# Kernel tuning notes

Measured on AMD Instinct MI355X. Metric: run time of the kernel, lower is better.

## Reference

```python
import jax, jax.numpy as jnp
import numpy as np

H = 28; W = 28; N = H * W
P = N              # padded max persistence pairs per homology dimension
T = 32             # landscape resolution
K1, K2 = 2, 3      # K_max for the two topo layers
M0_1, M0_2 = 0.05, 0.2
LIMS = ((1.0, 28.0), (1.0, 28.0))


def _make_nbrs(h, w, conn8):
    idx = np.arange(h * w).reshape(h, w)
    offs = [(-1, 0), (1, 0), (0, -1), (0, 1)]
    if conn8:
        offs += [(-1, -1), (-1, 1), (1, -1), (1, 1)]
    nbrs = []
    for i in range(h):
        for j in range(w):
            cur = [idx[i + a, j + b] for a, b in offs if 0 <= i + a < h and 0 <= j + b < w]
            nbrs.append(np.asarray(cur, np.int64))
    return nbrs

_NBR4 = _make_nbrs(H, W, False)
_NBR8 = _make_nbrs(H, W, True)


def _h0_pairs(vals, nbrs):
    # 0-dim persistence pairs of a vertex-valued sublevel filtration (union-find, elder rule)
    order = np.argsort(vals, kind="stable")
    pos = np.empty(N, np.int64); pos[order] = np.arange(N)
    parent = np.arange(N); birth = np.arange(N)
    added = np.zeros(N, bool)
    bi = np.zeros(P, np.int32); di = np.zeros(P, np.int32)
    k = 0
    def find(x):
        r = x
        while parent[r] != r: r = parent[r]
        while parent[x] != r: parent[x], x = r, parent[x]
        return r
    for v in order:
        added[v] = True
        for u in nbrs[v]:
            if not added[u]: continue
            ru, rv = find(u), find(v)
            if ru == rv: continue
            if pos[birth[ru]] <= pos[birth[rv]]:
                lb = birth[rv]; parent[rv] = ru
            else:
                lb = birth[ru]; parent[ru] = rv
            if k < P:
                bi[k] = lb; di[k] = v; k += 1
    return bi, di


def _pers_pairs_np(x):
    # x: [M, N] -> (birth_idx, death_idx) each [M, 2, P]; padded pairs point at idx 0 (zero persistence)
    x = np.asarray(x, np.float64)
    M = x.shape[0]
    bi = np.zeros((M, 2, P), np.int32); di = np.zeros((M, 2, P), np.int32)
    for m in range(M):
        b0, d0 = _h0_pairs(x[m], _NBR4)      # H0: sublevel, 4-connectivity
        b1, d1 = _h0_pairs(-x[m], _NBR8)     # H1 by Alexander duality: H0 of superlevel, 8-connectivity
        bi[m, 0], di[m, 0] = b0, d0
        bi[m, 1], di[m, 1] = d1, b1          # H1 birth = vals[d1], death = vals[b1]
    return bi, di


def _grid_d2():
    xs = np.linspace(LIMS[0][0], LIMS[0][1], H)
    ys = np.linspace(LIMS[1][0], LIMS[1][1], W)
    gx, gy = np.meshgrid(xs, ys, indexing="ij")
    pts = np.stack([gx.ravel(), gy.ravel()], 1)              # [N, 2] grid coordinates
    d2 = ((pts[:, None, :] - pts[None, :, :]) ** 2).sum(-1)  # [N, N] squared distances
    si = np.argsort(d2, axis=1, kind="stable")
    return jnp.asarray(si), jnp.asarray(np.take_along_axis(d2, si, 1), jnp.float32)

_SORT_IDX, _D2S = _grid_d2()


def dtm(x_flat, m0):
    # weighted distance-to-measure on the pixel grid, r=2; x_flat: [M, N] positive weights
    bound = m0 * jnp.sum(x_flat, -1, keepdims=True)                        # [M, 1]
    ws = x_flat[:, _SORT_IDX]                                              # [M, N, N] weights in distance order
    cum = jnp.cumsum(ws, -1)
    eff = jnp.minimum(jnp.maximum(bound[..., None] - (cum - ws), 0.0), ws) # effective mass per neighbor
    return jnp.sqrt(jnp.sum(eff * _D2S, -1) / bound)                       # [M, N]


def _landscape(vals, bi, di, start, end, K):
    # persistence landscape lambda_k sampled on T points from (birth, death) critical-vertex indices
    M = vals.shape[0]
    mi = jnp.arange(M)[:, None, None]
    b = vals[mi, bi]; d = vals[mi, di]                                     # [M, 2, P]
    t = jnp.linspace(start, end, T, dtype=vals.dtype)                      # [T]
    tent = jnp.maximum(jnp.minimum(t - b[..., None], d[..., None] - t), 0.0)  # [M, 2, P, T]
    lam, _ = jax.lax.top_k(jnp.swapaxes(tent, -1, -2), K)                  # [M, 2, T, K]
    return jnp.swapaxes(lam, -1, -2).reshape(M, 2 * K * T)                 # [M, dims*K*T]


def pl_features(vals, start, end, K):
    M = vals.shape[0]
    bi, di = jax.pure_callback(
        _pers_pairs_np,
        (jax.ShapeDtypeStruct((M, 2, P), np.int32),
         jax.ShapeDtypeStruct((M, 2, P), np.int32)),
        jax.lax.stop_gradient(vals))
    return _landscape(vals, bi, di, start, end, K)


def setup_inputs():
    key = jax.random.key(0)
    ks = jax.random.split(key, 7)
    B = 64
    return {
        "input": jax.random.uniform(ks[0], (B, 1, H, W), jnp.float32, 1e-3, 1.0),
        "w_g1": 0.1 * jax.random.normal(ks[1], (32, 2 * K1 * T), jnp.float32),
        "b_g1": 0.1 * jax.random.normal(ks[2], (32,), jnp.float32),
        "w_g2": 0.1 * jax.random.normal(ks[3], (32, 2 * K2 * T), jnp.float32),
        "b_g2": 0.1 * jax.random.normal(ks[4], (32,), jnp.float32),
        "w_fc": 0.1 * jax.random.normal(ks[5], (10, 64), jnp.float32),
        "b_fc": 0.1 * jax.random.normal(ks[6], (10,), jnp.float32),
    }


def reference(input, w_g1, b_g1, w_g2, b_g2, w_fc, b_fc):
    x_flat = input.reshape(-1, N)                                        # num_channels = 1
    f1 = dtm(x_flat, M0_1)
    f2 = dtm(x_flat, M0_2)
    x1 = jax.nn.relu(pl_features(f1, 0.0, 7.0, K1) @ w_g1.T + b_g1)      # topo layer 1 (start=0, end=7, K=2)
    x2 = jax.nn.relu(pl_features(f2, 1.0, 8.0, K2) @ w_g2.T + b_g2)      # topo layer 2 (start=1, end=8, K=3)
    return jnp.concatenate([x1, x2], -1) @ w_fc.T + b_fc                 # [B, num_classes]
```

## Files before the change

### kernel.cpp

```cpp
#include <hip/hip_runtime.h>

#define HW 28
#define NPIX 784
#define NIMG 64
#define MAXD2 1459
#define MAXREC 5504

#define DXPK 41048u
#define DYPK 34949u

__global__ void xt_sums_kernel(const float* __restrict__ x,
                               float* __restrict__ sums,
                               float* __restrict__ xT) {
    int tid = threadIdx.x;
    int m = blockIdx.x;
    const float* xr = x + m * NPIX;
    float acc = 0.f;
    for (int j = tid; j < NPIX; j += 256) {
        float v = xr[j];
        xT[j * NIMG + m] = v;
        acc += v;
    }
    for (int off = 32; off > 0; off >>= 1) acc += __shfl_down(acc, off, 64);
    __shared__ float red[4];
    int lane = tid & 63, w = tid >> 6;
    if (lane == 0) red[w] = acc;
    __syncthreads();
    if (tid == 0) sums[m] = red[0] + red[1] + red[2] + red[3];
}

__global__ void sortdtm_kernel(const float* __restrict__ x,
                               const float* __restrict__ xT,
                               const float* __restrict__ sums,
                               float* __restrict__ F) {
    __shared__ int cnt[MAXD2];
    __shared__ int d2v[NPIX];
    __shared__ unsigned int tpl[NPIX];
    __shared__ int wtot[4];
    int tid = threadIdx.x;
    int i = blockIdx.x;

    for (int b = tid; b < MAXD2; b += 256) cnt[b] = 0;
    __syncthreads();
    int ii = i / HW, ij = i % HW;
    for (int j = tid; j < NPIX; j += 256) {
        int di = ii - j / HW, dj = ij - j % HW;
        int d = di * di + dj * dj;
        d2v[j] = d;
        atomicAdd(&cnt[d], 1);
    }
    __syncthreads();
    int b0 = tid * 6;
    int lc[6];
    int s0 = 0;
    #pragma unroll
    for (int t = 0; t < 6; ++t) {
        int b = b0 + t;
        lc[t] = (b < MAXD2) ? cnt[b] : 0;
        s0 += lc[t];
    }
    int lane = tid & 63, wv = tid >> 6;
    int v = s0;
    for (int off = 1; off < 64; off <<= 1) {
        int t2 = __shfl_up(v, off, 64);
        if (lane >= off) v += t2;
    }
    if (lane == 63) wtot[wv] = v;
    __syncthreads();
    int wadd = 0;
    for (int w2 = 0; w2 < wv; ++w2) wadd += wtot[w2];
    int run = wadd + v - s0;
    __syncthreads();
    #pragma unroll
    for (int t = 0; t < 6; ++t) {
        int b = b0 + t;
        if (b < MAXD2) { cnt[b] = run; run += lc[t]; }
    }
    __syncthreads();
    for (int j = tid; j < NPIX; j += 256) {
        int d = d2v[j];
        int slot = atomicAdd(&cnt[d], 1);
        tpl[slot] = (unsigned)j | ((unsigned)d << 16);
    }
    __syncthreads();

    if (tid < 64) {
        float s = sums[tid];
        float bound1 = 0.05f * s, bound2 = 0.2f * s;
        float cum = 0.f, acc1 = 0.f, acc2 = 0.f;
        for (int t0 = 0; t0 < NPIX; t0 += 8) {
            unsigned int e[8];
            #pragma unroll
            for (int u = 0; u < 8; ++u) e[u] = tpl[t0 + u];
            float w[8];
            #pragma unroll
            for (int u = 0; u < 8; ++u) w[u] = xT[(e[u] & 0xffffu) * NIMG + tid];
            #pragma unroll
            for (int u = 0; u < 8; ++u) {
                float d2 = (float)(e[u] >> 16);
                float ce = cum;
                cum += w[u];
                acc1 += fminf(fmaxf(bound1 - ce, 0.f), w[u]) * d2;
                acc2 += fminf(fmaxf(bound2 - ce, 0.f), w[u]) * d2;
            }
            if (__ballot(cum < bound2) == 0ull) break;
        }
        F[0 * NIMG * NPIX + tid * NPIX + i] = sqrtf(acc1 / bound1);
        F[1 * NIMG * NPIX + tid * NPIX + i] = sqrtf(acc2 / bound2);
    }
}

template<int NN>
__device__ int uf_basin_run(const int* posA, const int* ordA,
                            int* bas, unsigned int* pb, int* comp,
                            int* recs, int* pairsI,
                            int2* mergeLDS, int* shInts, int* wtot16) {
    const int tid = threadIdx.x;
    const int lane = tid & 63, wv = tid >> 6;

    for (int s = tid; s < NPIX; s += 1024) {
        int si = s / HW, sj = s % HW;
        int bestPos = posA[s], best = s;
        #pragma unroll
        for (int o = 0; o < NN; ++o) {
            int dx = ((DXPK >> (2 * o)) & 3) - 1;
            int dy = ((DYPK >> (2 * o)) & 3) - 1;
            int ui = si + dx, uj = sj + dy;
            if ((unsigned)ui < (unsigned)HW && (unsigned)uj < (unsigned)HW) {
                int u = ui * HW + uj;
                int pu = posA[u];
                if (pu < bestPos) { bestPos = pu; best = u; }
            }
        }
        bas[s] = best;
    }
    __syncthreads();

    for (int it = 0; it < 10; ++it) {
        int changed = 0;
        for (int s = tid; s < NPIX; s += 1024) {
            int b = bas[s];
            int bb = bas[b];
            if (bb != b) { bas[s] = bb; changed = 1; }
        }
        if (__syncthreads_count(changed) == 0) break;
    }

    for (int s = tid; s < NPIX; s += 1024)
        pb[s] = ((unsigned)posA[s] << 10) | (unsigned)bas[s];
    __syncthreads();

    int nrec = 0;
    {
        int r = tid;
        int cnt = 0;
        int myr[NN - 1];
        int got[NN - 1];
        #pragma unroll
        for (int t = 0; t < NN - 1; ++t) { got[t] = -1; myr[t] = 0; }
        if (r > 0 && r < NPIX) {
            int v = ordA[r];
            int vi = v / HW, vj = v % HW;
            int pivot = (int)(pb[v] & 1023u);
            #pragma unroll
            for (int o = 0; o < NN; ++o) {
                int dx = ((DXPK >> (2 * o)) & 3) - 1;
                int dy = ((DYPK >> (2 * o)) & 3) - 1;
                int ui = vi + dx, uj = vj + dy;
                if ((unsigned)ui < (unsigned)HW && (unsigned)uj < (unsigned)HW) {
                    int u = ui * HW + uj;
                    unsigned e = pb[u];
                    if ((int)(e >> 10) < r) {
                        int b = (int)(e & 1023u);
                        bool dup = (b == pivot);
                        #pragma unroll
                        for (int t = 0; t < NN - 1; ++t) dup = dup || (got[t] == b);
                        if (!dup) {
                            #pragma unroll
                            for (int t = 0; t < NN - 1; ++t)
                                if (t == cnt) { got[t] = b; myr[t] = (v << 20) | (pivot << 10) | b; }
                            cnt++;
                        }
                    }
                }
            }
        }
        int p = cnt;
        for (int off = 1; off < 64; off <<= 1) {
            int t2 = __shfl_up(p, off, 64);
            if (lane >= off) p += t2;
        }
        if (lane == 63) wtot16[wv] = p;
        __syncthreads();
        int wadd = 0;
        for (int w2 = 0; w2 < wv; ++w2) wadd += wtot16[w2];
        int tot = 0;
        #pragma unroll
        for (int w2 = 0; w2 < 16; ++w2) tot += wtot16[w2];
        int excl = wadd + p - cnt;
        #pragma unroll
        for (int t = 0; t < NN - 1; ++t)
            if (t < cnt) recs[excl + t] = myr[t];
        nrec = tot;
        __syncthreads();
    }

    int k = 0;
    for (int base = 0; base < nrec; base += 64) {
        int nrem = 0;
        if (wv == 0) {
            int idx = base + lane;
            int rec = (idx < nrec) ? recs[idx] : 0;
            int pa = (rec >> 10) & 1023, pbn = rec & 1023;
            int ka = 0, kb = 0;
            if (idx < nrec) { ka = comp[pa]; kb = comp[pbn]; }
            for (;;) {
                unsigned long long d = __ballot(ka != kb);
                if (d == 0ull) break;
                int i = (int)__ffsll((long long)d) - 1;
                int sA = __builtin_amdgcn_readlane(ka, i);
                int sB = __builtin_amdgcn_readlane(kb, i);
                int w = min(sA, sB), l = max(sA, sB);
                int sv = __builtin_amdgcn_readlane(rec, i) >> 20;
                if (lane == 0) {
                    pairsI[k] = (l & 1023) | (sv << 10);
                    mergeLDS[nrem] = make_int2(l, w);
                }
                k++;
                ka = (ka == l) ? w : ka;
                kb = (kb == l) ? w : kb;
                nrem++;
                if (nrem == 63) {
                    for (int s = lane; s < NPIX; s += 64) {
                        int cv = comp[s], c0 = cv;
                        for (int e = 0; e < nrem; ++e) {
                            int2 me = mergeLDS[e];
                            cv = (cv == me.x) ? me.y : cv;
                        }
                        if (cv != c0) comp[s] = cv;
                    }
                    if (idx < nrec) { ka = comp[pa]; kb = comp[pbn]; }
                    nrem = 0;
                }
            }
            if (lane == 0) shInts[0] = nrem;
        }
        __syncthreads();
        int nr = shInts[0];
        if (nr > 0) {
            for (int s = tid; s < NPIX; s += 1024) {
                int cv = comp[s], c0 = cv;
                for (int e = 0; e < nr; ++e) {
                    int2 me = mergeLDS[e];
                    cv = (cv == me.x) ? me.y : cv;
                }
                if (cv != c0) comp[s] = cv;
            }
        }
        __syncthreads();
    }
    if (tid == 0) shInts[1] = k;
    __syncthreads();
    return shInts[1];
}

__global__ void __launch_bounds__(1024) uf_land_kernel(const float* __restrict__ F,
                                                       float* __restrict__ LAM1,
                                                       float* __restrict__ LAM2) {
    __shared__ int posA[NPIX], ordA[NPIX], bas[NPIX], comp[NPIX], pairsI[NPIX];
    __shared__ unsigned int pbArr[NPIX];
    __shared__ alignas(16) unsigned long long key64[NPIX];
    __shared__ float fv[NPIX];
    __shared__ int recs[MAXREC];
    __shared__ int2 mergeLDS[64];
    __shared__ int shInts[2];
    __shared__ int wtot16[16];
    int tid = threadIdx.x;
    int task = blockIdx.x;
    int feat = task >> 7;
    int dir = (task >> 6) & 1;
    int m = task & 63;
    const float* fr = F + feat * NIMG * NPIX + m * NPIX;

    for (int j = tid; j < NPIX; j += 1024) {
        float f = fr[j];
        fv[j] = f;
        unsigned int b = __float_as_uint(f);
        if (dir) b = ~b;
        key64[j] = ((unsigned long long)b << 10) | (unsigned)j;
    }
    __syncthreads();

    if (tid < NPIX) {
        unsigned long long pki = key64[tid];
        int rank = 0;
        const ulonglong2* k2 = (const ulonglong2*)key64;
        for (int c = 0; c < NPIX / 2; ++c) {
            ulonglong2 kv = k2[c];
            rank += (int)(kv.x < pki) + (int)(kv.y < pki);
        }
        posA[tid] = rank;
        ordA[rank] = tid;
    }
    __syncthreads();
    for (int s = tid; s < NPIX; s += 1024) comp[s] = (posA[s] << 10) | s;

    int k;
    if (dir == 0) k = uf_basin_run<4>(posA, ordA, bas, pbArr, comp, recs, pairsI,
                                      mergeLDS, shInts, wtot16);
    else          k = uf_basin_run<8>(posA, ordA, bas, pbArr, comp, recs, pairsI,
                                      mergeLDS, shInts, wtot16);

    if (tid < 32) {
        int t = tid;
        float start = (feat == 0) ? 0.f : 1.f;
        float end   = (feat == 0) ? 7.f : 8.f;
        float tv = start + (end - start) * ((float)t / 31.f);
        float v0 = 0.f, v1 = 0.f, v2 = 0.f;
        for (int p = 0; p < k; ++p) {
            int pi = pairsI[p];
            float fb = fv[pi & 1023], fd = fv[pi >> 10];
            float bb = dir ? fd : fb;
            float dd = dir ? fb : fd;
            float tent = fmaxf(fminf(tv - bb, dd - tv), 0.f);
            if (tent > v0)      { v2 = v1; v1 = v0; v0 = tent; }
            else if (tent > v1) { v2 = v1; v1 = tent; }
            else if (tent > v2) { v2 = tent; }
        }
        if (feat == 0) {
            float* lam = LAM1 + m * 128 + dir * 64;
            lam[0 * 32 + t] = v0;
            lam[1 * 32 + t] = v1;
        } else {
            float* lam = LAM2 + m * 192 + dir * 96;
            lam[0 * 32 + t] = v0;
            lam[1 * 32 + t] = v1;
            lam[2 * 32 + t] = v2;
        }
    }
}

__global__ void mlp_kernel(const float* __restrict__ LAM1, const float* __restrict__ LAM2,
                           const float* __restrict__ w1, const float* __restrict__ b1,
                           const float* __restrict__ w2, const float* __restrict__ b2,
                           const float* __restrict__ wf, const float* __restrict__ bf,
                           float* __restrict__ out) {
    __shared__ float xc[64];
    int m = blockIdx.x;
    int n = threadIdx.x;
    if (n < 32) {
        float acc = b1[n];
        const float* l = LAM1 + m * 128;
        for (int c = 0; c < 128; ++c) acc += w1[n * 128 + c] * l[c];
        xc[n] = fmaxf(acc, 0.f);
    } else {
        int n2 = n - 32;
        float acc = b2[n2];
        const float* l = LAM2 + m * 192;
        for (int c = 0; c < 192; ++c) acc += w2[n2 * 192 + c] * l[c];
        xc[n] = fmaxf(acc, 0.f);
    }
    __syncthreads();
    if (n < 10) {
        float acc = bf[n];
        for (int c = 0; c < 64; ++c) acc += wf[n * 64 + c] * xc[c];
        out[m * 10 + n] = acc;
    }
}

extern "C" void kernel_launch(void* const* d_in, const int* in_sizes, int n_in,
                              void* d_out, int out_size, void* d_ws, size_t ws_size,
                              hipStream_t stream) {
    const float* x  = (const float*)d_in[0];
    const float* w1 = (const float*)d_in[1];
    const float* b1 = (const float*)d_in[2];
    const float* w2 = (const float*)d_in[3];
    const float* b2 = (const float*)d_in[4];
    const float* wf = (const float*)d_in[5];
    const float* bf = (const float*)d_in[6];
    float* out = (float*)d_out;

    char* ws = (char*)d_ws;
    size_t off = 0;
    float* XT   = (float*)(ws + off); off += (size_t)NPIX * NIMG * 4;
    float* SUMS = (float*)(ws + off); off += 256;
    float* F    = (float*)(ws + off); off += (size_t)2 * NIMG * NPIX * 4;
    float* LAM1 = (float*)(ws + off); off += (size_t)NIMG * 128 * 4;
    float* LAM2 = (float*)(ws + off); off += (size_t)NIMG * 192 * 4;

    xt_sums_kernel<<<NIMG, 256, 0, stream>>>(x, SUMS, XT);
    sortdtm_kernel<<<NPIX, 256, 0, stream>>>(x, XT, SUMS, F);
    uf_land_kernel<<<256, 1024, 0, stream>>>(F, LAM1, LAM2);
    mlp_kernel<<<NIMG, 64, 0, stream>>>(LAM1, LAM2, w1, b1, w2, b2, wf, bf, out);
}
```

Baseline: 120.5 us.

## Replace per-pixel counting sort with presorted offset table and parallelize landscape top-k

Precomputes on the host a table of all (dx,dy) offsets sorted by squared distance. Each DTM block now filters that table to in-bounds neighbours and compacts them with a prefix scan, replacing the LDS histogram, atomics and counting sort. The landscape stage now spreads the pair scan across all 1024 threads with per-subgroup top-3 partials merged by 32 threads, instead of one warp looping over every pair. It adds a host-to-device copy of the table on every launch, and the partial buffer reuses the recs shared array.

```diff
diff --git a/kernel.cpp b/kernel.cpp
--- a/kernel.cpp
+++ b/kernel.cpp
@@ -1,13 +1,42 @@
 #include <hip/hip_runtime.h>
+#include <algorithm>
 
 #define HW 28
 #define NPIX 784
 #define NIMG 64
-#define MAXD2 1459
 #define MAXREC 5504
+#define NOFF 3025
+#define NOFFP 3072
 
 #define DXPK 41048u
 #define DYPK 34949u
+
+namespace {
+struct OffTbl {
+    unsigned int t[NOFFP];
+    OffTbl() {
+        struct E { int d2, lin, dx, dy; };
+        static E es[NOFF];
+        int n = 0;
+        for (int dx = -27; dx <= 27; ++dx)
+            for (int dy = -27; dy <= 27; ++dy) {
+                es[n].d2 = dx * dx + dy * dy;
+                es[n].lin = dx * HW + dy;
+                es[n].dx = dx; es[n].dy = dy;
+                ++n;
+            }
+        std::sort(es, es + NOFF, [](const E& a, const E& b) {
+            return a.d2 != b.d2 ? a.d2 < b.d2 : a.lin < b.lin;
+        });
+        for (int k2 = 0; k2 < NOFF; ++k2)
+            t[k2] = ((unsigned)es[k2].d2 << 16) |
+                    ((unsigned)(es[k2].dx + 27) << 8) |
+                    (unsigned)(es[k2].dy + 27);
+        for (int k2 = NOFF; k2 < NOFFP; ++k2) t[k2] = 0xFFFFFFFFu;
+    }
+};
+OffTbl g_offtbl;
+}
 
 __global__ void xt_sums_kernel(const float* __restrict__ x,
                                float* __restrict__ sums,
@@ -29,58 +58,47 @@
     if (tid == 0) sums[m] = red[0] + red[1] + red[2] + red[3];
 }
 
-__global__ void sortdtm_kernel(const float* __restrict__ x,
+__global__ void __launch_bounds__(256) sortdtm_kernel(const unsigned int* __restrict__ OTB,
                                const float* __restrict__ xT,
                                const float* __restrict__ sums,
                                float* __restrict__ F) {
-    __shared__ int cnt[MAXD2];
-    __shared__ int d2v[NPIX];
     __shared__ unsigned int tpl[NPIX];
     __shared__ int wtot[4];
     int tid = threadIdx.x;
     int i = blockIdx.x;
-
-    for (int b = tid; b < MAXD2; b += 256) cnt[b] = 0;
-    __syncthreads();
     int ii = i / HW, ij = i % HW;
-    for (int j = tid; j < NPIX; j += 256) {
-        int di = ii - j / HW, dj = ij - j % HW;
-        int d = di * di + dj * dj;
-        d2v[j] = d;
-        atomicAdd(&cnt[d], 1);
-    }
-    __syncthreads();
-    int b0 = tid * 6;
-    int lc[6];
-    int s0 = 0;
+
+    const uint4* o4 = (const uint4*)OTB + tid * 3;
+    uint4 qa = o4[0], qb = o4[1], qc = o4[2];
+    unsigned int ent[12] = {qa.x, qa.y, qa.z, qa.w,
+                            qb.x, qb.y, qb.z, qb.w,
+                            qc.x, qc.y, qc.z, qc.w};
+    int ct = 0;
     #pragma unroll
-    for (int t = 0; t < 6; ++t) {
-        int b = b0 + t;
-        lc[t] = (b < MAXD2) ? cnt[b] : 0;
-        s0 += lc[t];
+    for (int e = 0; e < 12; ++e) {
+        int dx = (int)((ent[e] >> 8) & 255u) - 27;
+        int dy = (int)(ent[e] & 255u) - 27;
+        ct += ((unsigned)(ii + dx) < (unsigned)HW && (unsigned)(ij + dy) < (unsigned)HW) ? 1 : 0;
     }
     int lane = tid & 63, wv = tid >> 6;
-    int v = s0;
+    int p = ct;
     for (int off = 1; off < 64; off <<= 1) {
-        int t2 = __shfl_up(v, off, 64);
-        if (lane >= off) v += t2;
-    }
-    if (lane == 63) wtot[wv] = v;
-    __syncthreads();
-    int wadd = 0;
-    for (int w2 = 0; w2 < wv; ++w2) wadd += wtot[w2];
-    int run = wadd + v - s0;
-    __syncthreads();
+        int t2 = __shfl_up(p, off, 64);
+        if (lane >= off) p += t2;
+    }
+    if (lane == 63) wtot[wv] = p;
+    __syncthreads();
+    int slot = p - ct;
+    for (int w2 = 0; w2 < wv; ++w2) slot += wtot[w2];
     #pragma unroll
-    for (int t = 0; t < 6; ++t) {
-        int b = b0 + t;
-        if (b < MAXD2) { cnt[b] = run; run += lc[t]; }
-    }
-    __syncthreads();
-    for (int j = tid; j < NPIX; j += 256) {
-        int d = d2v[j];
-        int slot = atomicAdd(&cnt[d], 1);
-        tpl[slot] = (unsigned)j | ((unsigned)d << 16);
+    for (int e = 0; e < 12; ++e) {
+        int dx = (int)((ent[e] >> 8) & 255u) - 27;
+        int dy = (int)(ent[e] & 255u) - 27;
+        int ui = ii + dx, uj = ij + dy;
+        if ((unsigned)ui < (unsigned)HW && (unsigned)uj < (unsigned)HW) {
+            tpl[slot] = (unsigned)(ui * HW + uj) | (ent[e] & 0xFFFF0000u);
+            ++slot;
+        }
     }
     __syncthreads();
 
@@ -271,7 +289,7 @@
     __shared__ unsigned int pbArr[NPIX];
     __shared__ alignas(16) unsigned long long key64[NPIX];
     __shared__ float fv[NPIX];
-    __shared__ int recs[MAXREC];
+    __shared__ alignas(16) int recs[MAXREC];
     __shared__ int2 mergeLDS[64];
     __shared__ int shInts[2];
     __shared__ int wtot16[16];
@@ -311,13 +329,14 @@
     else          k = uf_basin_run<8>(posA, ordA, bas, pbArr, comp, recs, pairsI,
                                       mergeLDS, shInts, wtot16);
 
-    if (tid < 32) {
-        int t = tid;
-        float start = (feat == 0) ? 0.f : 1.f;
-        float end   = (feat == 0) ? 7.f : 8.f;
+    float start = (feat == 0) ? 0.f : 1.f;
+    float end   = (feat == 0) ? 7.f : 8.f;
+    {
+        int sub = tid >> 5;
+        int t = tid & 31;
         float tv = start + (end - start) * ((float)t / 31.f);
         float v0 = 0.f, v1 = 0.f, v2 = 0.f;
-        for (int p = 0; p < k; ++p) {
+        for (int p = sub; p < k; p += 32) {
             int pi = pairsI[p];
             float fb = fv[pi & 1023], fd = fv[pi >> 10];
             float bb = dir ? fd : fb;
@@ -326,6 +345,25 @@
             if (tent > v0)      { v2 = v1; v1 = v0; v0 = tent; }
             else if (tent > v1) { v2 = v1; v1 = tent; }
             else if (tent > v2) { v2 = tent; }
+        }
+        float* part = (float*)recs;
+        int bse = (sub * 32 + t) * 3;
+        part[bse] = v0; part[bse + 1] = v1; part[bse + 2] = v2;
+    }
+    __syncthreads();
+    if (tid < 32) {
+        int t = tid;
+        const float* part = (const float*)recs;
+        float v0 = 0.f, v1 = 0.f, v2 = 0.f;
+        for (int s2 = 0; s2 < 32; ++s2) {
+            int bse = (s2 * 32 + t) * 3;
+            #pragma unroll
+            for (int q = 0; q < 3; ++q) {
+                float x = part[bse + q];
+                if (x > v0)      { v2 = v1; v1 = v0; v0 = x; }
+                else if (x > v1) { v2 = v1; v1 = x; }
+                else if (x > v2) { v2 = x; }
+            }
         }
         if (feat == 0) {
             float* lam = LAM1 + m * 128 + dir * 64;
@@ -382,14 +420,16 @@
 
     char* ws = (char*)d_ws;
     size_t off = 0;
+    unsigned int* OTB = (unsigned int*)(ws + off); off += (size_t)NOFFP * 4;
     float* XT   = (float*)(ws + off); off += (size_t)NPIX * NIMG * 4;
     float* SUMS = (float*)(ws + off); off += 256;
     float* F    = (float*)(ws + off); off += (size_t)2 * NIMG * NPIX * 4;
     float* LAM1 = (float*)(ws + off); off += (size_t)NIMG * 128 * 4;
     float* LAM2 = (float*)(ws + off); off += (size_t)NIMG * 192 * 4;
 
+    hipMemcpyAsync(OTB, g_offtbl.t, (size_t)NOFFP * 4, hipMemcpyHostToDevice, stream);
     xt_sums_kernel<<<NIMG, 256, 0, stream>>>(x, SUMS, XT);
-    sortdtm_kernel<<<NPIX, 256, 0, stream>>>(x, XT, SUMS, F);
+    sortdtm_kernel<<<NPIX, 256, 0, stream>>>(OTB, XT, SUMS, F);
     uf_land_kernel<<<256, 1024, 0, stream>>>(F, LAM1, LAM2);
     mlp_kernel<<<NIMG, 64, 0, stream>>>(LAM1, LAM2, w1, b1, w2, b2, wf, bf, out);
 }
```

Measured after the change: 127.8 us. 1.06x slower.
